# Performance work log

Hardware: AMD Instinct MI355X
Metric: run time of the kernel (lower is better)

## Reference

```python
import jax, jax.numpy as jnp
import numpy as np

N_E = 1024
E_DIM = 64
BETA = 0.25


def setup_inputs() -> dict:
    key = jax.random.key(0)
    k1, k2 = jax.random.split(key)
    z = jax.random.normal(k1, (16, E_DIM, 64, 64), dtype=jnp.float32)
    # embedding initialized uniform(-1/n_e, 1/n_e) as in the torch module
    emb = jax.random.uniform(k2, (N_E, E_DIM), dtype=jnp.float32,
                             minval=-1.0 / N_E, maxval=1.0 / N_E)
    return {"z": z, "emb": emb}


def reference(z, emb):
    n_e, e_dim = emb.shape
    # NCHW -> NHWC, flatten to tokens
    zp = jnp.transpose(z, (0, 2, 3, 1))            # [B,H,W,C]
    zf = zp.reshape(-1, e_dim)                      # [N,C]
    # squared distances ||zf||^2 + ||e||^2 - 2 zf e^T  -> [N, n_e]
    d = (jnp.sum(zf * zf, axis=1, keepdims=True)
         + jnp.sum(emb * emb, axis=1)
         - 2.0 * jnp.matmul(zf, emb.T))
    idx = jnp.argmin(d, axis=1)                     # [N]
    # one-hot @ emb is exactly a gather
    z_q = emb[idx].reshape(zp.shape)                # [B,H,W,C]
    loss = (jnp.mean((jax.lax.stop_gradient(z_q) - zp) ** 2)
            + BETA * jnp.mean((z_q - jax.lax.stop_gradient(zp)) ** 2))
    # straight-through estimator
    z_q = zp + jax.lax.stop_gradient(z_q - zp)
    # perplexity from codeword usage histogram
    counts = jax.ops.segment_sum(jnp.ones_like(idx, dtype=zf.dtype), idx,
                                 num_segments=n_e)
    e_mean = counts / zf.shape[0]
    perplexity = jnp.exp(-jnp.sum(e_mean * jnp.log(e_mean + 1e-10)))
    min_encoding_indices = idx.reshape(z.shape[0], -1).astype(jnp.int32)
    z_q = jnp.transpose(z_q, (0, 3, 1, 2))          # back to NCHW
    return z_q, loss, perplexity, min_encoding_indices
```

## Files before the change

kernel.cpp:

```cpp
#include <hip/hip_runtime.h>

#define TOKS 65536
#define ED 64
#define NE 1024
#define CH_STRIDE 4096
#define B_STRIDE 262144

typedef __bf16 bf16x8 __attribute__((ext_vector_type(8)));
typedef float f32x16 __attribute__((ext_vector_type(16)));
typedef unsigned short ushort_t;
typedef unsigned int uint_t;


__device__ __forceinline__ ushort_t f2bf(float x) {
    uint_t u = __float_as_uint(x);
    uint_t r = u + 0x7FFFu + ((u >> 16) & 1u);
    return (ushort_t)(r >> 16);
}

__global__ __launch_bounds__(256) void vq_prep_e(const float* __restrict__ emb,
                                                 ushort_t* __restrict__ efrag,
                                                 float* __restrict__ enorm,
                                                 int* __restrict__ hist,
                                                 double* __restrict__ lossAcc) {
    const int tid = threadIdx.x;
    const int w = tid >> 6, lane = tid & 63;
    const int j = blockIdx.x * 4 + w;

    const float e = emb[j * 64 + lane];
    const float sq = __fmul_rn(e, e);
    float acc = sq;
    acc = __fadd_rn(acc, __shfl_down(sq, 8, 64));
    acc = __fadd_rn(acc, __shfl_down(sq, 16, 64));
    acc = __fadd_rn(acc, __shfl_down(sq, 24, 64));
    acc = __fadd_rn(acc, __shfl_down(sq, 32, 64));
    acc = __fadd_rn(acc, __shfl_down(sq, 40, 64));
    acc = __fadd_rn(acc, __shfl_down(sq, 48, 64));
    acc = __fadd_rn(acc, __shfl_down(sq, 56, 64));
    float x = __fadd_rn(acc, __shfl_down(acc, 1, 64));
    float y = __fadd_rn(x, __shfl_down(x, 2, 64));
    float zn = __fadd_rn(y, __shfl_down(y, 4, 64));
    if (lane == 0) enorm[j] = zn;

    const ushort_t h = f2bf(-2.0f * e);
    const int ct = j >> 5, m = j & 31;
    const int ks = lane >> 4, kh = (lane >> 3) & 1, i = lane & 7;
    efrag[(size_t)((ct * 4 + ks) * 512) + (m + 32 * kh) * 8 + i] = h;

    if (blockIdx.x < 4) hist[blockIdx.x * 256 + tid] = 0;
    if (blockIdx.x == 0 && tid == 0) *lossAcc = 0.0;
}

__global__ __launch_bounds__(256, 4) void vq_main(
    const float* __restrict__ z,
    const ushort_t* __restrict__ efrag,
    const float* __restrict__ enorm,
    const float* __restrict__ emb,
    float* __restrict__ zq,
    float* __restrict__ out_idx,
    int* __restrict__ hist,
    double* __restrict__ lossAcc) {
    __shared__ float z_s[64][36];
    __shared__ uint_t skey[4][32][2][3];
    __shared__ float s_zn[32];
    __shared__ unsigned long long s_res[32];
    __shared__ uint_t s_cand[128];
    __shared__ int s_cnt;
    __shared__ double wsum[4];

    const int tid = threadIdx.x;
    const int w = tid >> 6, lane = tid & 63;
    const int t0 = blockIdx.x * 32;
    const int b = t0 >> 12, hw0 = t0 & 4095;
    const float* zbase = z + (size_t)b * B_STRIDE + hw0;

    {
        const int c = tid >> 2, u0 = (tid & 3) * 8;
        const float* src = zbase + (size_t)c * CH_STRIDE + u0;
        float4 f0 = *(const float4*)(src);
        float4 f1 = *(const float4*)(src + 4);
        *(float4*)&z_s[c][u0] = f0;
        *(float4*)&z_s[c][u0 + 4] = f1;
    }
    if (tid < 32) s_res[tid] = 0xFFFFFFFFFFFFFFFFull;
    if (tid == 0) s_cnt = 0;

    const int n = lane & 31, kh = lane >> 5;

    bf16x8 zb[4];
    #pragma unroll
    for (int ks = 0; ks < 4; ++ks) {
        #pragma unroll
        for (int i = 0; i < 8; ++i) {
            union { ushort_t u; __bf16 bh; } ca;
            ca.u = f2bf(zbase[(size_t)(ks * 16 + kh * 8 + i) * CH_STRIDE + n]);
            zb[ks][i] = ca.bh;
        }
    }

    uint_t k0 = 0xFFFFFFFFu, k1 = 0xFFFFFFFFu, k2 = 0xFFFFFFFFu;
    const bf16x8* eg = (const bf16x8*)efrag;

    #pragma unroll
    for (int ct = 0; ct < 8; ++ct) {
        const int gct = w * 8 + ct;
        bf16x8 ah0 = eg[(size_t)(gct * 4 + 0) * 64 + lane];
        bf16x8 ah1 = eg[(size_t)(gct * 4 + 1) * 64 + lane];
        bf16x8 ah2 = eg[(size_t)(gct * 4 + 2) * 64 + lane];
        bf16x8 ah3 = eg[(size_t)(gct * 4 + 3) * 64 + lane];

        f32x16 acc;
        #pragma unroll
        for (int r = 0; r < 16; ++r) acc[r] = 0.25f;
        acc = __builtin_amdgcn_mfma_f32_32x32x16_bf16(ah0, zb[0], acc, 0, 0, 0);
        acc = __builtin_amdgcn_mfma_f32_32x32x16_bf16(ah1, zb[1], acc, 0, 0, 0);
        acc = __builtin_amdgcn_mfma_f32_32x32x16_bf16(ah2, zb[2], acc, 0, 0, 0);
        acc = __builtin_amdgcn_mfma_f32_32x32x16_bf16(ah3, zb[3], acc, 0, 0, 0);

        const int jb = gct * 32 + 4 * kh;
        #pragma unroll
        for (int r = 0; r < 16; ++r) {
            uint_t key = (__float_as_uint(acc[r]) & 0xFFFFFC00u)
                         | (uint_t)(jb + (r & 3) + 8 * (r >> 2));
            uint_t mx = max(k0, key);
            k2 = min(k2, max(k1, mx));
            k1 = min(k1, mx);
            k0 = min(k0, key);
        }
    }

    skey[w][n][kh][0] = k0; skey[w][n][kh][1] = k1; skey[w][n][kh][2] = k2;
    __syncthreads();

    const int t_loc = tid >> 3, m = tid & 7;
    {
        float a = z_s[m][t_loc];
        float racc = __fmul_rn(a, a);
        #pragma unroll
        for (int i = 1; i < 8; ++i) {
            float av = z_s[m + 8 * i][t_loc];
            racc = __fadd_rn(racc, __fmul_rn(av, av));
        }
        float x1 = __fadd_rn(racc, __shfl_xor(racc, 1, 64));
        float y1 = __fadd_rn(x1, __shfl_xor(x1, 2, 64));
        float zn = __fadd_rn(y1, __shfl_xor(y1, 4, 64));
        if (m == 0) s_zn[t_loc] = zn;
    }
    {
        uint_t ck[3];
        #pragma unroll
        for (int s = 0; s < 3; ++s) ck[s] = skey[m >> 1][t_loc][m & 1][s];
        uint_t kmin = min(ck[0], min(ck[1], ck[2]));
        kmin = min(kmin, (uint_t)__shfl_xor((int)kmin, 1, 64));
        kmin = min(kmin, (uint_t)__shfl_xor((int)kmin, 2, 64));
        kmin = min(kmin, (uint_t)__shfl_xor((int)kmin, 4, 64));
        const float thr = __uint_as_float(kmin & 0xFFFFFC00u) + 4.0e-4f;
        #pragma unroll
        for (int s = 0; s < 3; ++s) {
            if (__uint_as_float(ck[s] & 0xFFFFFC00u) <= thr) {
                int pos = atomicAdd(&s_cnt, 1);
                if (pos < 128)
                    s_cand[pos] = ((uint_t)t_loc << 10) | (ck[s] & 1023u);
            }
        }
    }
    __syncthreads();

    {
        const int cnt = s_cnt;
        if (tid < cnt && tid < 128) {
            const uint_t cd = s_cand[tid];
            const int tok = (int)(cd >> 10), j = (int)(cd & 1023u);
            const float* e = emb + (size_t)j * 64;
            float a0 = 0.f;
            #pragma unroll
            for (int k4 = 0; k4 < 64; k4 += 4) {
                float4 e4 = *(const float4*)(e + k4);
                a0 = __fmaf_rn(z_s[k4 + 0][tok], e4.x, a0);
                a0 = __fmaf_rn(z_s[k4 + 1][tok], e4.y, a0);
                a0 = __fmaf_rn(z_s[k4 + 2][tok], e4.z, a0);
                a0 = __fmaf_rn(z_s[k4 + 3][tok], e4.w, a0);
            }
            float d = __fsub_rn(__fadd_rn(s_zn[tok], enorm[j]), 2.0f * a0);
            unsigned long long key =
                ((unsigned long long)__float_as_uint(d) << 10)
                | (unsigned long long)j;
            atomicMin(&s_res[tok], key);
        }
    }
    __syncthreads();

    const int bj = (int)(s_res[t_loc] & 1023u);
    if (m == 0) {
        out_idx[t0 + t_loc] = (float)bj;
        atomicAdd(&hist[bj], 1);
    }
    double ls = 0.0;
    {
        const float* e = emb + (size_t)bj * 64;
        #pragma unroll
        for (int i = 0; i < 8; ++i) {
            const int k = m + 8 * i;
            float ev = e[k];
            float zv = z_s[k][t_loc];
            z_s[k][t_loc] = ev;
            float df = ev - zv;
            ls += (double)(df * df);
        }
    }
    #pragma unroll
    for (int off = 32; off > 0; off >>= 1) ls += __shfl_down(ls, off, 64);
    if (lane == 0) wsum[w] = ls;
    __syncthreads();
    if (tid == 0)
        atomicAdd(lossAcc, wsum[0] + wsum[1] + wsum[2] + wsum[3]);

    {
        const int c = tid >> 2, u0 = (tid & 3) * 8;
        float4 f0 = *(const float4*)&z_s[c][u0];
        float4 f1 = *(const float4*)&z_s[c][u0 + 4];
        float* dst = zq + (size_t)b * B_STRIDE + (size_t)c * CH_STRIDE + hw0 + u0;
        *(float4*)(dst) = f0;
        *(float4*)(dst + 4) = f1;
    }
}

__global__ __launch_bounds__(256) void vq_final(const int* __restrict__ hist,
                                                const double* __restrict__ lossAcc,
                                                float* __restrict__ outs) {
    __shared__ double red[256];
    double acc = 0.0;
    for (int j = threadIdx.x; j < NE; j += 256) {
        double em = (double)hist[j] * (1.0 / 65536.0);
        acc += em * log(em + 1e-10);
    }
    red[threadIdx.x] = acc;
    __syncthreads();
    for (int s = 128; s > 0; s >>= 1) {
        if (threadIdx.x < s) red[threadIdx.x] += red[threadIdx.x + s];
        __syncthreads();
    }
    if (threadIdx.x == 0) {
        outs[0] = (float)(1.25 * (*lossAcc) * (1.0 / 4194304.0));
        outs[1] = (float)exp(-red[0]);
    }
}

extern "C" void kernel_launch(void* const* d_in, const int* in_sizes, int n_in,
                              void* d_out, int out_size, void* d_ws, size_t ws_size,
                              hipStream_t stream) {
    const float* z = (const float*)d_in[0];
    const float* emb = (const float*)d_in[1];
    float* out = (float*)d_out;

    char* ws = (char*)d_ws;
    ushort_t* efrag = (ushort_t*)ws;
    float* enorm = (float*)(ws + 131072);
    int* hist = (int*)(ws + 135168);
    double* lossAcc = (double*)(ws + 139264);

    float* zq = out;
    float* scalars = out + 4194304;
    float* out_idx = out + 4194306;

    vq_prep_e<<<256, 256, 0, stream>>>(emb, efrag, enorm, hist, lossAcc);
    vq_main<<<2048, 256, 0, stream>>>(z, efrag, enorm, emb, zq, out_idx, hist, lossAcc);
    vq_final<<<1, 256, 0, stream>>>(hist, lossAcc, scalars);
}
```

Measured before the change: 49.23 us.

## Restructure VQ main kernel: token-major smem, prefetched codebook tiles, top-2 candidates, partial loss sums

```diff
diff --git a/kernel.cpp b/kernel.cpp
--- a/kernel.cpp
+++ b/kernel.cpp
@@ -21,8 +21,7 @@
 __global__ __launch_bounds__(256) void vq_prep_e(const float* __restrict__ emb,
                                                  ushort_t* __restrict__ efrag,
                                                  float* __restrict__ enorm,
-                                                 int* __restrict__ hist,
-                                                 double* __restrict__ lossAcc) {
+                                                 int* __restrict__ hist) {
     const int tid = threadIdx.x;
     const int w = tid >> 6, lane = tid & 63;
     const int j = blockIdx.x * 4 + w;
@@ -48,7 +47,6 @@
     efrag[(size_t)((ct * 4 + ks) * 512) + (m + 32 * kh) * 8 + i] = h;
 
     if (blockIdx.x < 4) hist[blockIdx.x * 256 + tid] = 0;
-    if (blockIdx.x == 0 && tid == 0) *lossAcc = 0.0;
 }
 
 __global__ __launch_bounds__(256, 4) void vq_main(
@@ -59,13 +57,10 @@
     float* __restrict__ zq,
     float* __restrict__ out_idx,
     int* __restrict__ hist,
-    double* __restrict__ lossAcc) {
-    __shared__ float z_s[64][36];
-    __shared__ uint_t skey[4][32][2][3];
-    __shared__ float s_zn[32];
+    double* __restrict__ lossPart) {
+    __shared__ float z_s[32][68];
+    __shared__ uint_t skey[4][32][2];
     __shared__ unsigned long long s_res[32];
-    __shared__ uint_t s_cand[128];
-    __shared__ int s_cnt;
     __shared__ double wsum[4];
 
     const int tid = threadIdx.x;
@@ -79,35 +74,50 @@
         const float* src = zbase + (size_t)c * CH_STRIDE + u0;
         float4 f0 = *(const float4*)(src);
         float4 f1 = *(const float4*)(src + 4);
-        *(float4*)&z_s[c][u0] = f0;
-        *(float4*)&z_s[c][u0 + 4] = f1;
+        z_s[u0 + 0][c] = f0.x; z_s[u0 + 1][c] = f0.y;
+        z_s[u0 + 2][c] = f0.z; z_s[u0 + 3][c] = f0.w;
+        z_s[u0 + 4][c] = f1.x; z_s[u0 + 5][c] = f1.y;
+        z_s[u0 + 6][c] = f1.z; z_s[u0 + 7][c] = f1.w;
     }
     if (tid < 32) s_res[tid] = 0xFFFFFFFFFFFFFFFFull;
-    if (tid == 0) s_cnt = 0;
+    __syncthreads();
 
     const int n = lane & 31, kh = lane >> 5;
 
     bf16x8 zb[4];
     #pragma unroll
     for (int ks = 0; ks < 4; ++ks) {
+        float4 a0 = *(const float4*)&z_s[n][ks * 16 + kh * 8];
+        float4 a1 = *(const float4*)&z_s[n][ks * 16 + kh * 8 + 4];
+        const float av[8] = {a0.x, a0.y, a0.z, a0.w, a1.x, a1.y, a1.z, a1.w};
         #pragma unroll
         for (int i = 0; i < 8; ++i) {
-            union { ushort_t u; __bf16 bh; } ca;
-            ca.u = f2bf(zbase[(size_t)(ks * 16 + kh * 8 + i) * CH_STRIDE + n]);
-            zb[ks][i] = ca.bh;
-        }
-    }
-
-    uint_t k0 = 0xFFFFFFFFu, k1 = 0xFFFFFFFFu, k2 = 0xFFFFFFFFu;
+            union { ushort_t u; __bf16 bh; } cv;
+            cv.u = f2bf(av[i]);
+            zb[ks][i] = cv.bh;
+        }
+    }
+
+    uint_t k0 = 0xFFFFFFFFu, k1 = 0xFFFFFFFFu;
     const bf16x8* eg = (const bf16x8*)efrag;
-
-    #pragma unroll
+    const int rot = blockIdx.x & 7;
+
+    int gct = w * 8 + rot;
+    bf16x8 ah0 = eg[(size_t)(gct * 4 + 0) * 64 + lane];
+    bf16x8 ah1 = eg[(size_t)(gct * 4 + 1) * 64 + lane];
+    bf16x8 ah2 = eg[(size_t)(gct * 4 + 2) * 64 + lane];
+    bf16x8 ah3 = eg[(size_t)(gct * 4 + 3) * 64 + lane];
+
     for (int ct = 0; ct < 8; ++ct) {
-        const int gct = w * 8 + ct;
-        bf16x8 ah0 = eg[(size_t)(gct * 4 + 0) * 64 + lane];
-        bf16x8 ah1 = eg[(size_t)(gct * 4 + 1) * 64 + lane];
-        bf16x8 ah2 = eg[(size_t)(gct * 4 + 2) * 64 + lane];
-        bf16x8 ah3 = eg[(size_t)(gct * 4 + 3) * 64 + lane];
+        const int gnext = w * 8 + ((ct + 1 + rot) & 7);
+        bf16x8 nx0, nx1, nx2, nx3;
+        if (ct < 7) {
+            nx0 = eg[(size_t)(gnext * 4 + 0) * 64 + lane];
+            nx1 = eg[(size_t)(gnext * 4 + 1) * 64 + lane];
+            nx2 = eg[(size_t)(gnext * 4 + 2) * 64 + lane];
+            nx3 = eg[(size_t)(gnext * 4 + 3) * 64 + lane];
+        }
+        const int jb = gct * 32 + 4 * kh;
 
         f32x16 acc;
         #pragma unroll
@@ -117,108 +127,108 @@
         acc = __builtin_amdgcn_mfma_f32_32x32x16_bf16(ah2, zb[2], acc, 0, 0, 0);
         acc = __builtin_amdgcn_mfma_f32_32x32x16_bf16(ah3, zb[3], acc, 0, 0, 0);
 
-        const int jb = gct * 32 + 4 * kh;
         #pragma unroll
         for (int r = 0; r < 16; ++r) {
             uint_t key = (__float_as_uint(acc[r]) & 0xFFFFFC00u)
                          | (uint_t)(jb + (r & 3) + 8 * (r >> 2));
             uint_t mx = max(k0, key);
-            k2 = min(k2, max(k1, mx));
             k1 = min(k1, mx);
             k0 = min(k0, key);
         }
-    }
-
-    skey[w][n][kh][0] = k0; skey[w][n][kh][1] = k1; skey[w][n][kh][2] = k2;
-    __syncthreads();
-
-    const int t_loc = tid >> 3, m = tid & 7;
-    {
-        float a = z_s[m][t_loc];
+        ah0 = nx0; ah1 = nx1; ah2 = nx2; ah3 = nx3;
+        gct = gnext;
+    }
+
+    {
+        uint_t p0 = (uint_t)__shfl_xor((int)k0, 32, 64);
+        uint_t p1 = (uint_t)__shfl_xor((int)k1, 32, 64);
+        uint_t o0 = min(k0, p0);
+        uint_t o1 = min(max(k0, p0), min(k1, p1));
+        if (kh == 0) { skey[w][n][0] = o0; skey[w][n][1] = o1; }
+    }
+    __syncthreads();
+
+    const int tok = tid >> 3, p = tid & 7;
+    const uint_t ck = skey[p >> 1][tok][p & 1];
+    uint_t kmin = ck;
+    kmin = min(kmin, (uint_t)__shfl_xor((int)kmin, 1, 64));
+    kmin = min(kmin, (uint_t)__shfl_xor((int)kmin, 2, 64));
+    kmin = min(kmin, (uint_t)__shfl_xor((int)kmin, 4, 64));
+    const float thr = __uint_as_float(kmin & 0xFFFFFC00u) + 4.0e-4f;
+
+    float zn;
+    {
+        float a = z_s[tok][p];
         float racc = __fmul_rn(a, a);
         #pragma unroll
         for (int i = 1; i < 8; ++i) {
-            float av = z_s[m + 8 * i][t_loc];
+            float av = z_s[tok][p + 8 * i];
             racc = __fadd_rn(racc, __fmul_rn(av, av));
         }
         float x1 = __fadd_rn(racc, __shfl_xor(racc, 1, 64));
         float y1 = __fadd_rn(x1, __shfl_xor(x1, 2, 64));
-        float zn = __fadd_rn(y1, __shfl_xor(y1, 4, 64));
-        if (m == 0) s_zn[t_loc] = zn;
-    }
-    {
-        uint_t ck[3];
-        #pragma unroll
-        for (int s = 0; s < 3; ++s) ck[s] = skey[m >> 1][t_loc][m & 1][s];
-        uint_t kmin = min(ck[0], min(ck[1], ck[2]));
-        kmin = min(kmin, (uint_t)__shfl_xor((int)kmin, 1, 64));
-        kmin = min(kmin, (uint_t)__shfl_xor((int)kmin, 2, 64));
-        kmin = min(kmin, (uint_t)__shfl_xor((int)kmin, 4, 64));
-        const float thr = __uint_as_float(kmin & 0xFFFFFC00u) + 4.0e-4f;
-        #pragma unroll
-        for (int s = 0; s < 3; ++s) {
-            if (__uint_as_float(ck[s] & 0xFFFFFC00u) <= thr) {
-                int pos = atomicAdd(&s_cnt, 1);
-                if (pos < 128)
-                    s_cand[pos] = ((uint_t)t_loc << 10) | (ck[s] & 1023u);
-            }
-        }
-    }
-    __syncthreads();
-
-    {
-        const int cnt = s_cnt;
-        if (tid < cnt && tid < 128) {
-            const uint_t cd = s_cand[tid];
-            const int tok = (int)(cd >> 10), j = (int)(cd & 1023u);
-            const float* e = emb + (size_t)j * 64;
-            float a0 = 0.f;
-            #pragma unroll
-            for (int k4 = 0; k4 < 64; k4 += 4) {
-                float4 e4 = *(const float4*)(e + k4);
-                a0 = __fmaf_rn(z_s[k4 + 0][tok], e4.x, a0);
-                a0 = __fmaf_rn(z_s[k4 + 1][tok], e4.y, a0);
-                a0 = __fmaf_rn(z_s[k4 + 2][tok], e4.z, a0);
-                a0 = __fmaf_rn(z_s[k4 + 3][tok], e4.w, a0);
-            }
-            float d = __fsub_rn(__fadd_rn(s_zn[tok], enorm[j]), 2.0f * a0);
-            unsigned long long key =
-                ((unsigned long long)__float_as_uint(d) << 10)
-                | (unsigned long long)j;
-            atomicMin(&s_res[tok], key);
-        }
-    }
-    __syncthreads();
-
-    const int bj = (int)(s_res[t_loc] & 1023u);
-    if (m == 0) {
-        out_idx[t0 + t_loc] = (float)bj;
+        zn = __fadd_rn(y1, __shfl_xor(y1, 4, 64));
+    }
+
+    if (__uint_as_float(ck & 0xFFFFFC00u) <= thr) {
+        const int j = (int)(ck & 1023u);
+        const float* e = emb + (size_t)j * 64;
+        float a0 = 0.f;
+        #pragma unroll
+        for (int k4 = 0; k4 < 16; ++k4) {
+            float4 z4 = *(const float4*)&z_s[tok][k4 * 4];
+            float4 e4 = *(const float4*)(e + k4 * 4);
+            a0 = __fmaf_rn(z4.x, e4.x, a0);
+            a0 = __fmaf_rn(z4.y, e4.y, a0);
+            a0 = __fmaf_rn(z4.z, e4.z, a0);
+            a0 = __fmaf_rn(z4.w, e4.w, a0);
+        }
+        float d = __fsub_rn(__fadd_rn(zn, enorm[j]), 2.0f * a0);
+        unsigned long long key =
+            ((unsigned long long)__float_as_uint(d) << 10)
+            | (unsigned long long)j;
+        atomicMin(&s_res[tok], key);
+    }
+    __syncthreads();
+
+    const int bj = (int)(s_res[tok] & 1023u);
+    if (p == 0) {
+        out_idx[t0 + tok] = (float)bj;
         atomicAdd(&hist[bj], 1);
     }
     double ls = 0.0;
     {
-        const float* e = emb + (size_t)bj * 64;
-        #pragma unroll
-        for (int i = 0; i < 8; ++i) {
-            const int k = m + 8 * i;
-            float ev = e[k];
-            float zv = z_s[k][t_loc];
-            z_s[k][t_loc] = ev;
-            float df = ev - zv;
-            ls += (double)(df * df);
-        }
+        const float* e = emb + (size_t)bj * 64 + p * 8;
+        float4 e0 = *(const float4*)(e);
+        float4 e1 = *(const float4*)(e + 4);
+        float4 zv0 = *(const float4*)&z_s[tok][p * 8];
+        float4 zv1 = *(const float4*)&z_s[tok][p * 8 + 4];
+        float df;
+        df = e0.x - zv0.x; ls += (double)(df * df);
+        df = e0.y - zv0.y; ls += (double)(df * df);
+        df = e0.z - zv0.z; ls += (double)(df * df);
+        df = e0.w - zv0.w; ls += (double)(df * df);
+        df = e1.x - zv1.x; ls += (double)(df * df);
+        df = e1.y - zv1.y; ls += (double)(df * df);
+        df = e1.z - zv1.z; ls += (double)(df * df);
+        df = e1.w - zv1.w; ls += (double)(df * df);
+        *(float4*)&z_s[tok][p * 8] = e0;
+        *(float4*)&z_s[tok][p * 8 + 4] = e1;
     }
     #pragma unroll
     for (int off = 32; off > 0; off >>= 1) ls += __shfl_down(ls, off, 64);
     if (lane == 0) wsum[w] = ls;
     __syncthreads();
     if (tid == 0)
-        atomicAdd(lossAcc, wsum[0] + wsum[1] + wsum[2] + wsum[3]);
+        lossPart[blockIdx.x] = wsum[0] + wsum[1] + wsum[2] + wsum[3];
 
     {
         const int c = tid >> 2, u0 = (tid & 3) * 8;
-        float4 f0 = *(const float4*)&z_s[c][u0];
-        float4 f1 = *(const float4*)&z_s[c][u0 + 4];
+        float4 f0, f1;
+        f0.x = z_s[u0 + 0][c]; f0.y = z_s[u0 + 1][c];
+        f0.z = z_s[u0 + 2][c]; f0.w = z_s[u0 + 3][c];
+        f1.x = z_s[u0 + 4][c]; f1.y = z_s[u0 + 5][c];
+        f1.z = z_s[u0 + 6][c]; f1.w = z_s[u0 + 7][c];
         float* dst = zq + (size_t)b * B_STRIDE + (size_t)c * CH_STRIDE + hw0 + u0;
         *(float4*)(dst) = f0;
         *(float4*)(dst + 4) = f1;
@@ -226,22 +236,29 @@
 }
 
 __global__ __launch_bounds__(256) void vq_final(const int* __restrict__ hist,
-                                                const double* __restrict__ lossAcc,
+                                                const double* __restrict__ lossPart,
                                                 float* __restrict__ outs) {
     __shared__ double red[256];
+    __shared__ double red2[256];
     double acc = 0.0;
     for (int j = threadIdx.x; j < NE; j += 256) {
         double em = (double)hist[j] * (1.0 / 65536.0);
         acc += em * log(em + 1e-10);
     }
+    double lsum = 0.0;
+    for (int j = threadIdx.x; j < 2048; j += 256) lsum += lossPart[j];
     red[threadIdx.x] = acc;
+    red2[threadIdx.x] = lsum;
     __syncthreads();
     for (int s = 128; s > 0; s >>= 1) {
-        if (threadIdx.x < s) red[threadIdx.x] += red[threadIdx.x + s];
+        if (threadIdx.x < s) {
+            red[threadIdx.x] += red[threadIdx.x + s];
+            red2[threadIdx.x] += red2[threadIdx.x + s];
+        }
         __syncthreads();
     }
     if (threadIdx.x == 0) {
-        outs[0] = (float)(1.25 * (*lossAcc) * (1.0 / 4194304.0));
+        outs[0] = (float)(1.25 * red2[0] * (1.0 / 4194304.0));
         outs[1] = (float)exp(-red[0]);
     }
 }
@@ -257,13 +274,14 @@
     ushort_t* efrag = (ushort_t*)ws;
     float* enorm = (float*)(ws + 131072);
     int* hist = (int*)(ws + 135168);
-    double* lossAcc = (double*)(ws + 139264);
+    double* lossPart = (double*)(ws + 143360);
 
     float* zq = out;
     float* scalars = out + 4194304;
     float* out_idx = out + 4194306;
 
-    vq_prep_e<<<256, 256, 0, stream>>>(emb, efrag, enorm, hist, lossAcc);
-    vq_main<<<2048, 256, 0, stream>>>(z, efrag, enorm, emb, zq, out_idx, hist, lossAcc);
-    vq_final<<<1, 256, 0, stream>>>(hist, lossAcc, scalars);
-}
+    vq_prep_e<<<256, 256, 0, stream>>>(emb, efrag, enorm, hist);
+    vq_main<<<2048, 256, 0, stream>>>(z, efrag, enorm, emb, zq, out_idx,
+                                      hist, lossPart);
+    vq_final<<<1, 256, 0, stream>>>(hist, lossPart, scalars);
+}
```

Measured after the change: 45.26 us. -8.1%, faster.
